# Kernel tuning notes

Hardware: AMD Instinct MI355X
Metric: run time of the kernel (lower is better)

Reference implementation:

```python
import jax, jax.numpy as jnp
import numpy as np

G, N, H = 64, 512, 64          # graphs, nodes/graph, hidden
NT = G * N                     # total nodes
DEG = 32
ET = NT * DEG                  # total edges
KP = int(np.ceil(0.7 * N))     # TopKPooling keep per graph (359)
NP2 = G * KP                   # nodes after pooling
F_IN, NC, NA = 128, 2, 6
seg = jax.ops.segment_sum


def graph_norm(h, batch, num_g, w, b, ms, eps=1e-5):
    cnt = seg(jnp.ones((h.shape[0], 1), h.dtype), batch, num_segments=num_g)
    mean = seg(h, batch, num_segments=num_g) / cnt
    hc = h - ms * mean[batch]
    var = seg(hc * hc, batch, num_segments=num_g) / cnt
    return w * hc / jnp.sqrt(var[batch] + eps) + b


def sage(h, src, tgt, valid, Ws, Wn, b, n_nodes):
    # PyG SAGEConv (mean aggr): out_i = x_i@Ws + mean_{j->i} x_j @ Wn + b
    msg = h[src] * valid[:, None]
    agg = seg(msg, tgt, num_segments=n_nodes)
    deg = seg(valid, tgt, num_segments=n_nodes)
    return h @ Ws + (agg / jnp.maximum(deg, 1.0)[:, None]) @ Wn + b


def setup_inputs() -> dict:
    key = jax.random.key(0)
    ks = jax.random.split(key, 20)
    offs = (jnp.arange(G) * N)[:, None]
    src = (jax.random.randint(ks[0], (G, N * DEG), 0, N) + offs).reshape(-1)
    tgt = (jax.random.randint(ks[1], (G, N * DEG), 0, N) + offs).reshape(-1)
    edge_index = jnp.stack([src, tgt])  # within-graph edges

    def lin(k, fi, fo):
        return jax.random.normal(k, (fi, fo), jnp.float32) / np.sqrt(fi)

    return {
        "x": jax.random.normal(ks[2], (NT, F_IN), jnp.float32),
        "edge_index": edge_index,
        "edge_attr": jax.random.uniform(ks[3], (ET,), jnp.float32),
        "coords": jax.random.normal(ks[4], (NT, 3), jnp.float32),
        "anatomical_class": jax.random.randint(ks[5], (NT,), 0, NA),
        "Bk_table": jax.random.normal(ks[6], (NA, H * H), jnp.float32) * 0.05,
        "pos_W": lin(ks[7], 3, H), "pos_b": jnp.zeros((H,), jnp.float32),
        "W1_self": lin(ks[8], F_IN, H), "W1_neigh": lin(ks[9], F_IN, H),
        "b1": jnp.zeros((H,), jnp.float32),
        "gn1_w": jnp.ones((H,), jnp.float32), "gn1_b": jnp.zeros((H,), jnp.float32),
        "gn1_ms": jnp.ones((H,), jnp.float32),
        "pool_p": jax.random.normal(ks[10], (H,), jnp.float32),
        "W2_self": lin(ks[11], H, H), "W2_neigh": lin(ks[12], H, H),
        "b2": jnp.zeros((H,), jnp.float32),
        "gn2_w": jnp.ones((H,), jnp.float32), "gn2_b": jnp.zeros((H,), jnp.float32),
        "gn2_ms": jnp.ones((H,), jnp.float32),
        "lin1_W": lin(ks[13], 3 * H, H), "lin1_b": jnp.zeros((H,), jnp.float32),
        "lin2_W": lin(ks[14], H, NC), "lin2_b": jnp.zeros((NC,), jnp.float32),
    }


def reference(x, edge_index, edge_attr, coords, anatomical_class, Bk_table,
              pos_W, pos_b, W1_self, W1_neigh, b1, gn1_w, gn1_b, gn1_ms,
              pool_p, W2_self, W2_neigh, b2, gn2_w, gn2_b, gn2_ms,
              lin1_W, lin1_b, lin2_W, lin2_b):
    row, col = edge_index[0], edge_index[1]
    batch = jnp.repeat(jnp.arange(G), N)
    # ---- stage 1: anatomical propagation kernel ----
    e = coords @ pos_W + pos_b                                 # [NT, H]
    Ae = seg(edge_attr[:, None] * e[col], row, num_segments=NT)  # SpMM adj @ e
    Bk = Bk_table[anatomical_class].reshape(NT, H, H)
    delta = jnp.einsum('nd,nhd->nh', Ae, Bk)                   # bmm(Ae, Bk^T)
    ones_e = jnp.ones((ET,), x.dtype)
    h = sage(x, row, col, ones_e, W1_self, W1_neigh, b1, NT)
    h = jax.nn.elu(graph_norm(h, batch, G, gn1_w, gn1_b, gn1_ms))
    h = h + delta
    h = jnp.einsum('nij,nj->ni', Bk + delta[:, :, None], h)    # propagate_message
    # ---- TopK pooling (equal-sized graphs) ----
    score = (h @ pool_p) / jnp.linalg.norm(pool_p)
    vals, idx = jax.lax.top_k(score.reshape(G, N), KP)
    perm = (idx + (jnp.arange(G) * N)[:, None]).reshape(-1)    # [NP2]
    h = h[perm] * jnp.tanh(vals).reshape(-1)[:, None]
    batch2 = jnp.repeat(jnp.arange(G), KP)
    node_map = jnp.full((NT,), -1, jnp.int32).at[perm].set(jnp.arange(NP2, dtype=jnp.int32))
    s2, t2 = node_map[row], node_map[col]
    valid = ((s2 >= 0) & (t2 >= 0)).astype(h.dtype)            # masked edge filter
    s2 = jnp.where(s2 >= 0, s2, 0)
    t2 = jnp.where(t2 >= 0, t2, 0)
    # ---- stage 2 ----
    e2 = coords[perm] @ pos_W + pos_b
    Bk2 = Bk_table[anatomical_class[perm]].reshape(NP2, H, H)
    Ae2 = seg(valid[:, None] * e2[t2], s2, num_segments=NP2)   # edge_attr = ones
    delta2 = jnp.einsum('nd,nhd->nh', Ae2, Bk2)
    h = h + delta2
    h = jnp.einsum('nij,nj->ni', Bk2 + delta2[:, :, None], h)
    h = sage(h, s2, t2, valid, W2_self, W2_neigh, b2, NP2)
    h = jax.nn.elu(graph_norm(h, batch2, G, gn2_w, gn2_b, gn2_ms))
    # ---- readout ----
    cnt = seg(jnp.ones((NP2, 1), h.dtype), batch2, num_segments=G)
    hsum = seg(h, batch2, num_segments=G)
    g = jnp.concatenate([hsum / cnt,
                         jax.ops.segment_max(h, batch2, num_segments=G),
                         hsum], axis=1)
    g = jax.nn.relu(g @ lin1_W + lin1_b)
    return jax.nn.log_softmax(g @ lin2_W + lin2_b, axis=1)
```

## Files before the change

kernel.cpp:

```cpp
#include <hip/hip_runtime.h>
#include <math.h>

#define G_    64
#define N_    512
#define H_    64
#define NT_   32768
#define ET_   1048576
#define EPG_  16384
#define KP_   359
#define NP2_  22976
#define FIN_  128
#define ESL_  2048
#define BPB_  (EPG_/ESL_)

__global__ void k_prep(const float* __restrict__ Bk, const float* __restrict__ posW,
                       const float* __restrict__ posb,
                       float* __restrict__ BkT, float* __restrict__ PT) {
    int b = blockIdx.x, t = threadIdx.x;
    if (b < 96) {
        int idx = b * 256 + t;
        int c = idx >> 12, r = idx & 4095;
        int h = r >> 6, d = r & 63;
        BkT[c * 4096 + d * 64 + h] = Bk[c * 4096 + h * 64 + d];
    } else {
        int c = b - 96;
        int i = t >> 6, h = t & 63;
        const float* B = Bk + c * 4096 + h * 64;
        float acc = 0.f;
        for (int d = 0; d < 64; d++) {
            float vd = (i < 3) ? posW[i*64 + d] : posb[d];
            acc += B[d] * vd;
        }
        PT[c*256 + i*64 + h] = acc;
    }
}

__global__ __launch_bounds__(256)
void k_hist(const int* __restrict__ row, const int* __restrict__ col,
            int* __restrict__ histR, int* __restrict__ histC) {
    __shared__ int hr[N_], hc[N_];
    int b = blockIdx.x, g = b >> 3, s = b & (BPB_ - 1);
    int t = threadIdx.x;
    for (int i = t; i < N_; i += 256) { hr[i] = 0; hc[i] = 0; }
    __syncthreads();
    int ebase = g * EPG_ + s * ESL_;
    for (int i = t; i < ESL_; i += 256) {
        atomicAdd(&hr[row[ebase + i] & (N_ - 1)], 1);
        atomicAdd(&hc[col[ebase + i] & (N_ - 1)], 1);
    }
    __syncthreads();
    int nbase = g * N_;
    for (int i = t; i < N_; i += 256) {
        if (hr[i]) atomicAdd(&histR[nbase + i], hr[i]);
        if (hc[i]) atomicAdd(&histC[nbase + i], hc[i]);
    }
}

__global__ __launch_bounds__(256)
void k_scan(const int* __restrict__ histR, const int* __restrict__ histC,
            int* __restrict__ rowptr, int* __restrict__ colptr,
            float* __restrict__ deg, int* __restrict__ nmap) {
    __shared__ int hr[N_], hc[N_];
    int g = blockIdx.x, t = threadIdx.x;
    int nbase = g * N_;
    for (int i = t; i < N_; i += 256) {
        hr[i] = histR[nbase + i];
        int c = histC[nbase + i];
        hc[i] = c;
        deg[nbase + i] = (float)c;
        nmap[nbase + i] = -1;
    }
    __syncthreads();
    int wave = t >> 6, lane = t & 63;
    if (wave < 2) {
        int* h = wave ? hc : hr;
        int base8 = lane * 8;
        int loc[8];
        int tot = 0;
        #pragma unroll
        for (int i = 0; i < 8; i++) { int v = h[base8 + i]; loc[i] = tot; tot += v; }
        int pref = tot;
        for (int off = 1; off < 64; off <<= 1) {
            int u = __shfl_up(pref, off);
            if (lane >= off) pref += u;
        }
        pref -= tot;
        #pragma unroll
        for (int i = 0; i < 8; i++) h[base8 + i] = pref + loc[i];
    }
    __syncthreads();
    int ebase = g * EPG_;
    for (int i = t; i < N_; i += 256) {
        rowptr[nbase + i] = ebase + hr[i];
        colptr[nbase + i] = ebase + hc[i];
    }
    if (g == 0 && t == 0) { rowptr[NT_] = ET_; colptr[NT_] = ET_; }
}

__global__ __launch_bounds__(1024)
void k_scat(const int* __restrict__ row, const int* __restrict__ col,
            const float* __restrict__ ea,
            const int* __restrict__ rowptr, const int* __restrict__ colptr,
            int2* __restrict__ rowcsr, int* __restrict__ colcsr) {
    __shared__ int curR[128], curC[128];
    int g = blockIdx.x >> 2, q = blockIdx.x & 3;
    int t = threadIdx.x;
    int lo = q * 128;
    int nbase = g * N_ + lo;
    if (t < 128) { curR[t] = rowptr[nbase + t]; curC[t] = colptr[nbase + t]; }
    __syncthreads();
    int ebase = g * EPG_;
    for (int i = t; i < EPG_; i += 1024) {
        int rg = row[ebase + i];
        int cg = col[ebase + i];
        int rl = (rg & (N_ - 1)) - lo;
        if ((unsigned)rl < 128u) {
            int pr = atomicAdd(&curR[rl], 1);
            rowcsr[pr] = make_int2(cg, __float_as_int(ea[ebase + i]));
        }
        int cl = (cg & (N_ - 1)) - lo;
        if ((unsigned)cl < 128u) {
            int pc = atomicAdd(&curC[cl], 1);
            colcsr[pc] = rg;
        }
    }
}

__global__ __launch_bounds__(256)
void k_gemm_dual(const float* __restrict__ in, int K,
                 const float* __restrict__ Wa, const float* __restrict__ Wb,
                 const float* __restrict__ bias, const int* __restrict__ permA,
                 float* __restrict__ outA, float* __restrict__ outB) {
    __shared__ float inT[32 * FIN_];
    int row0 = blockIdx.x * 32;
    int t = threadIdx.x;
    for (int idx = t; idx < 32 * K; idx += 256) inT[idx] = in[row0 * K + idx];
    __syncthreads();
    int c = t & 63, rb = t >> 6;
    const float* ip = inT + (rb * 8) * K;
    float aA[8] = {0,0,0,0,0,0,0,0};
    float aB[8] = {0,0,0,0,0,0,0,0};
    for (int k = 0; k < K; k += 4) {
        float wa0 = Wa[(k+0)*64 + c], wa1 = Wa[(k+1)*64 + c];
        float wa2 = Wa[(k+2)*64 + c], wa3 = Wa[(k+3)*64 + c];
        float wb0 = Wb[(k+0)*64 + c], wb1 = Wb[(k+1)*64 + c];
        float wb2 = Wb[(k+2)*64 + c], wb3 = Wb[(k+3)*64 + c];
        #pragma unroll
        for (int r = 0; r < 8; r++) {
            float4 xv = *(const float4*)&ip[r*K + k];
            aA[r] += xv.x*wa0; aB[r] += xv.x*wb0;
            aA[r] += xv.y*wa1; aB[r] += xv.y*wb1;
            aA[r] += xv.z*wa2; aB[r] += xv.z*wb2;
            aA[r] += xv.w*wa3; aB[r] += xv.w*wb3;
        }
    }
    float bv = bias[c];
    #pragma unroll
    for (int r = 0; r < 8; r++) {
        int node = row0 + rb*8 + r;
        int rowA = permA ? permA[node] : node;
        outA[rowA*64 + c] = aA[r];
        outB[node*64 + c] = aB[r] + bv;
    }
}

__global__ __launch_bounds__(256)
void k_edge1f(const int* __restrict__ rowptr, const int2* __restrict__ rcsr,
              const int* __restrict__ colptr, const int* __restrict__ ccsr,
              const float* __restrict__ coords, const float* __restrict__ y,
              float4* __restrict__ nsum, float* __restrict__ agg) {
    int node = blockIdx.x * 4 + (threadIdx.x >> 6);
    int lane = threadIdx.x & 63;
    int rs = rowptr[node], re = rowptr[node + 1];
    float sx = 0.f, sy = 0.f, sz = 0.f, sw = 0.f;
    for (int k = rs + lane; k < re; k += 64) {
        int2 ent = rcsr[k];
        int c = ent.x;
        float w = __int_as_float(ent.y);
        sx += w * coords[c*3+0];
        sy += w * coords[c*3+1];
        sz += w * coords[c*3+2];
        sw += w;
    }
    #pragma unroll
    for (int off = 32; off; off >>= 1) {
        sx += __shfl_xor(sx, off); sy += __shfl_xor(sy, off);
        sz += __shfl_xor(sz, off); sw += __shfl_xor(sw, off);
    }
    if (lane == 0) nsum[node] = make_float4(sx, sy, sz, sw);
    int cs = colptr[node], ce = colptr[node + 1];
    float acc = 0.f;
    #pragma unroll 8
    for (int k = cs; k < ce; k++) {
        int r = ccsr[k];
        acc += y[r*64 + lane];
    }
    agg[node*64 + lane] = acc;
}

__global__ __launch_bounds__(256)
void k_gnstat(const float* __restrict__ hs, const float* __restrict__ agg,
              const float* __restrict__ deg, float* __restrict__ partial,
              int NPG, int CH, int npc) {
    __shared__ float r1[256], r2[256];
    int b = blockIdx.x;
    int g = b / CH, chunk = b % CH;
    int t = threadIdx.x, c = t & 63, grp = t >> 6;
    int n0 = chunk * npc;
    int nend = min(n0 + npc, NPG);
    float s1 = 0.f, s2 = 0.f;
    for (int n = n0 + grp; n < nend; n += 4) {
        int node = g * NPG + n;
        float v = hs[node*64 + c] + agg[node*64 + c] / fmaxf(deg[node], 1.f);
        s1 += v; s2 += v * v;
    }
    r1[t] = s1; r2[t] = s2;
    __syncthreads();
    if (grp == 0) {
        partial[b*128 + c]      = r1[c] + r1[64+c] + r1[128+c] + r1[192+c];
        partial[b*128 + 64 + c] = r2[c] + r2[64+c] + r2[128+c] + r2[192+c];
    }
}

__global__ void k_gnfin(const float* __restrict__ partial, const float* __restrict__ ms,
                        int CH, int NPG,
                        float* __restrict__ mval, float* __restrict__ istdv) {
    int g = blockIdx.x, t = threadIdx.x;
    float s1 = 0.f, s2 = 0.f;
    for (int i = 0; i < CH; i++) {
        s1 += partial[(g*CH + i)*128 + t];
        s2 += partial[(g*CH + i)*128 + 64 + t];
    }
    float m = s1 / (float)NPG, q = s2 / (float)NPG, msv = ms[t];
    float var = q - msv * m * m * (2.f - msv);
    mval[g*64 + t]  = msv * m;
    istdv[g*64 + t] = rsqrtf(var + 1e-5f);
}

__global__ __launch_bounds__(256)
void k_gnprop(const float* __restrict__ hself, const float* __restrict__ agg,
              const float* __restrict__ deg,
              const float* __restrict__ mval, const float* __restrict__ istdv,
              const float* __restrict__ w, const float* __restrict__ b,
              const float4* __restrict__ nsum, const int* __restrict__ cls,
              const float* __restrict__ PT, const float* __restrict__ BkT,
              float* __restrict__ out) {
    __shared__ float hT[256];
    int t = threadIdx.x;
    int node = blockIdx.x * 4 + (t >> 6);
    int lane = t & 63;
    int g = node >> 9;
    float4 s4 = nsum[node];
    int c = cls[node];
    const float* P = PT + c * 256;
    float d = s4.x*P[lane] + s4.y*P[64+lane] + s4.z*P[128+lane] + s4.w*P[192+lane];
    float v = hself[node*64 + lane] + agg[node*64 + lane] / fmaxf(deg[node], 1.f);
    v = w[lane] * (v - mval[g*64 + lane]) * istdv[g*64 + lane] + b[lane];
    v = v > 0.f ? v : expm1f(v);
    v += d;
    hT[t] = v;
    __syncthreads();
    float ssum = v;
    #pragma unroll
    for (int off = 32; off; off >>= 1) ssum += __shfl_xor(ssum, off);
    const float* B  = BkT + c * 4096;
    const float* hv = hT + (t & ~63);
    float acc = 0.f;
    #pragma unroll 8
    for (int j = 0; j < 64; j++) acc += B[j*64 + lane] * hv[j];
    out[node*64 + lane] = acc + d * ssum;
}

__global__ void k_topk(const float* __restrict__ hp, const float* __restrict__ p,
                       const int* __restrict__ cls,
                       int* __restrict__ perm, float* __restrict__ tanhv,
                       int* __restrict__ node_map, int* __restrict__ class2) {
    __shared__ float key[N_];
    __shared__ int   idxS[N_];
    __shared__ float pS[64];
    __shared__ float nrm;
    int g = blockIdx.x, t = threadIdx.x;
    if (t < 64) pS[t] = p[t];
    __syncthreads();
    if (t == 0) {
        float s = 0.f;
        for (int i = 0; i < 64; i++) s += pS[i] * pS[i];
        nrm = sqrtf(s);
    }
    __syncthreads();
    {
        float acc = 0.f;
        const float* hv = hp + (size_t)(g*N_ + t) * 64;
        for (int cdx = 0; cdx < 64; cdx++) acc += hv[cdx] * pS[cdx];
        key[t]  = acc / nrm;
        idxS[t] = t;
    }
    __syncthreads();
    for (int k = 2; k <= N_; k <<= 1) {
        for (int j = k >> 1; j > 0; j >>= 1) {
            int i = t, ixj = i ^ j;
            if (ixj > i) {
                float ki = key[i], kj = key[ixj];
                int   ii = idxS[i], ij = idxS[ixj];
                bool before = (ki > kj) || (ki == kj && ii < ij);
                bool dir = ((i & k) == 0);
                if (dir ? !before : before) {
                    key[i] = kj; key[ixj] = ki;
                    idxS[i] = ij; idxS[ixj] = ii;
                }
            }
            __syncthreads();
        }
    }
    if (t < KP_) {
        int orig  = idxS[t];
        int gnode = g * N_ + orig;
        int pj    = g * KP_ + t;
        perm[pj]     = gnode;
        tanhv[pj]    = tanhf(key[t]);
        node_map[gnode] = pj;
        class2[pj]   = cls[gnode];
    }
}

__global__ __launch_bounds__(256)
void k_s2prop(const int* __restrict__ rowptr, const int2* __restrict__ rcsr,
              const int* __restrict__ colptr, const int* __restrict__ ccsr,
              const int* __restrict__ perm, const int* __restrict__ nmap,
              const float* __restrict__ coords,
              const float* __restrict__ hp, const float* __restrict__ tanhv,
              const int* __restrict__ cls2,
              const float* __restrict__ PT, const float* __restrict__ BkT,
              float* __restrict__ out, float* __restrict__ deg2) {
    __shared__ float hT[256];
    int t = threadIdx.x;
    int j = blockIdx.x * 4 + (t >> 6);
    int lane = t & 63;
    int orig = perm[j];
    int rs = rowptr[orig], re = rowptr[orig + 1];
    float sx = 0.f, sy = 0.f, sz = 0.f, sw = 0.f;
    for (int k = rs + lane; k < re; k += 64) {
        int c = rcsr[k].x;
        if (nmap[c] >= 0) {
            sx += coords[c*3+0]; sy += coords[c*3+1]; sz += coords[c*3+2];
            sw += 1.f;
        }
    }
    int cs = colptr[orig], ce = colptr[orig + 1];
    float dg = 0.f;
    for (int k = cs + lane; k < ce; k += 64) {
        if (nmap[ccsr[k]] >= 0) dg += 1.f;
    }
    #pragma unroll
    for (int off = 32; off; off >>= 1) {
        sx += __shfl_xor(sx, off); sy += __shfl_xor(sy, off);
        sz += __shfl_xor(sz, off); sw += __shfl_xor(sw, off);
        dg += __shfl_xor(dg, off);
    }
    if (lane == 0) deg2[j] = dg;
    int c = cls2[j];
    const float* P = PT + c * 256;
    float d = sx*P[lane] + sy*P[64+lane] + sz*P[128+lane] + sw*P[192+lane];
    float v = hp[orig*64 + lane] * tanhv[j] + d;
    hT[t] = v;
    __syncthreads();
    float ssum = v;
    #pragma unroll
    for (int off = 32; off; off >>= 1) ssum += __shfl_xor(ssum, off);
    const float* B  = BkT + c * 4096;
    const float* hv = hT + (t & ~63);
    float acc = 0.f;
    #pragma unroll 8
    for (int jj = 0; jj < 64; jj++) acc += B[jj*64 + lane] * hv[jj];
    out[j*64 + lane] = acc + d * ssum;
}

__global__ __launch_bounds__(256)
void k_gagg2(const int* __restrict__ colptr, const int* __restrict__ ccsr,
             const int* __restrict__ perm, const float* __restrict__ y2full,
             float* __restrict__ agg2) {
    int j = blockIdx.x * 4 + (threadIdx.x >> 6);
    int lane = threadIdx.x & 63;
    int orig = perm[j];
    int start = colptr[orig], end = colptr[orig + 1];
    float acc = 0.f;
    #pragma unroll 8
    for (int k = start; k < end; k++) {
        int r = ccsr[k];
        acc += y2full[r*64 + lane];
    }
    agg2[j*64 + lane] = acc;
}

__global__ __launch_bounds__(256)
void k_gnrd(const float* __restrict__ hs, const float* __restrict__ agg,
            const float* __restrict__ deg2,
            const float* __restrict__ mval, const float* __restrict__ istdv,
            const float* __restrict__ w, const float* __restrict__ b,
            float* __restrict__ part, int CH, int npc) {
    __shared__ float r1[256], r2[256];
    int blk = blockIdx.x;
    int g = blk / CH, chunk = blk % CH;
    int t = threadIdx.x, c = t & 63, grp = t >> 6;
    int n0 = chunk * npc, nend = min(n0 + npc, KP_);
    float mv = mval[g*64 + c], is = istdv[g*64 + c], wv = w[c], bv = b[c];
    float s = 0.f, m = -1e30f;
    for (int n = n0 + grp; n < nend; n += 4) {
        int node = g * KP_ + n;
        float v = hs[node*64 + c] + agg[node*64 + c] / fmaxf(deg2[node], 1.f);
        v = wv * (v - mv) * is + bv;
        v = v > 0.f ? v : expm1f(v);
        s += v; m = fmaxf(m, v);
    }
    r1[t] = s; r2[t] = m;
    __syncthreads();
    if (grp == 0) {
        part[blk*128 + c]      = r1[c] + r1[64+c] + r1[128+c] + r1[192+c];
        part[blk*128 + 64 + c] = fmaxf(fmaxf(r2[c], r2[64+c]), fmaxf(r2[128+c], r2[192+c]));
    }
}

__global__ void k_rfin(const float* __restrict__ part, int CH,
                       const float* __restrict__ l1W, const float* __restrict__ l1b,
                       const float* __restrict__ l2W, const float* __restrict__ l2b,
                       float* __restrict__ out) {
    __shared__ float gv[192], rS[64];
    int g = blockIdx.x, t = threadIdx.x;
    float s = 0.f, m = -1e30f;
    for (int i = 0; i < CH; i++) {
        s += part[(g*CH + i)*128 + t];
        m = fmaxf(m, part[(g*CH + i)*128 + 64 + t]);
    }
    gv[t] = s / (float)KP_;
    gv[64 + t] = m;
    gv[128 + t] = s;
    __syncthreads();
    float acc = l1b[t];
    for (int k = 0; k < 192; k++) acc += gv[k] * l1W[k*64 + t];
    rS[t] = fmaxf(acc, 0.f);
    __syncthreads();
    if (t == 0) {
        float l0 = l2b[0], l1v = l2b[1];
        for (int hh = 0; hh < 64; hh++) { l0 += rS[hh]*l2W[hh*2+0]; l1v += rS[hh]*l2W[hh*2+1]; }
        float mx  = fmaxf(l0, l1v);
        float lse = mx + logf(expf(l0 - mx) + expf(l1v - mx));
        out[g*2 + 0] = l0  - lse;
        out[g*2 + 1] = l1v - lse;
    }
}

extern "C" void kernel_launch(void* const* d_in, const int* in_sizes, int n_in,
                              void* d_out, int out_size, void* d_ws, size_t ws_size,
                              hipStream_t stream) {
    const float* x      = (const float*)d_in[0];
    const int*   eidx   = (const int*)  d_in[1];
    const float* eattr  = (const float*)d_in[2];
    const float* coords = (const float*)d_in[3];
    const int*   acls   = (const int*)  d_in[4];
    const float* BkTab  = (const float*)d_in[5];
    const float* posW   = (const float*)d_in[6];
    const float* posb   = (const float*)d_in[7];
    const float* W1s    = (const float*)d_in[8];
    const float* W1n    = (const float*)d_in[9];
    const float* b1     = (const float*)d_in[10];
    const float* gn1w   = (const float*)d_in[11];
    const float* gn1b   = (const float*)d_in[12];
    const float* gn1ms  = (const float*)d_in[13];
    const float* poolp  = (const float*)d_in[14];
    const float* W2s    = (const float*)d_in[15];
    const float* W2n    = (const float*)d_in[16];
    const float* b2     = (const float*)d_in[17];
    const float* gn2w   = (const float*)d_in[18];
    const float* gn2b   = (const float*)d_in[19];
    const float* gn2ms  = (const float*)d_in[20];
    const float* l1W    = (const float*)d_in[21];
    const float* l1b    = (const float*)d_in[22];
    const float* l2W    = (const float*)d_in[23];
    const float* l2b    = (const float*)d_in[24];

    const int* row  = eidx;
    const int* colp = eidx + ET_;

    float* W = (float*)d_ws;
    const size_t NTH = (size_t)NT_ * 64;
    float* b0    = W;
    float* b1buf = W + 1*NTH;
    float* b2buf = W + 2*NTH;
    float* b3buf = W + 3*NTH;
    float* p = W + 4*NTH;
    int2*  rowcsr = (int2*)p;        p += 2*(size_t)ET_;
    int*   colcsr = (int*)p;         p += ET_;
    int*   rowptr = (int*)p;         p += NT_ + 8;
    int*   colptr = (int*)p;         p += NT_ + 8;
    int*   histR  = (int*)p;         p += NT_;
    int*   histC  = (int*)p;         p += NT_;
    float* deg    = p;               p += NT_;
    float* deg2   = p;               p += NP2_;
    float* tanhv  = p;               p += NP2_;
    int*   perm   = (int*)p;         p += NP2_;
    int*   nmap   = (int*)p;         p += NT_;
    int*   cls2   = (int*)p;         p += NP2_;
    float* BkT    = p;               p += 6 * 4096;
    float* PT     = p;               p += 6 * 256;
    float* meanv  = p;               p += G_ * 64;
    float* istdv  = p;               p += G_ * 64;
    float* partial= p;               p += (size_t)G_ * 8 * 128;
    float4* nsum  = (float4*)b3buf;

    hipMemsetAsync(histR, 0, 2 * NT_ * sizeof(int), stream);
    k_prep     <<<102,     256,  0, stream>>>(BkTab, posW, posb, BkT, PT);
    k_hist     <<<G_*BPB_, 256,  0, stream>>>(row, colp, histR, histC);
    k_scan     <<<G_,      256,  0, stream>>>(histR, histC, rowptr, colptr, deg, nmap);
    k_scat     <<<G_*4,    1024, 0, stream>>>(row, colp, eattr, rowptr, colptr,
                                              rowcsr, colcsr);

    k_gemm_dual<<<NT_/32,  256, 0, stream>>>(x, FIN_, W1n, W1s, b1, nullptr,
                                             b0 , b1buf );
    k_edge1f   <<<NT_/4,   256, 0, stream>>>(rowptr, rowcsr, colptr, colcsr,
                                             coords, b0 , nsum, b2buf );
    k_gnstat   <<<G_*8,    256, 0, stream>>>(b1buf , b2buf , deg,
                                             partial, N_, 8, 64);
    k_gnfin    <<<G_,      64,  0, stream>>>(partial, gn1ms, 8, N_, meanv, istdv);
    k_gnprop   <<<NT_/4,   256, 0, stream>>>(b1buf , b2buf , deg,
                                             meanv, istdv, gn1w, gn1b,
                                             nsum, acls, PT, BkT,
                                             b1buf );
    k_topk     <<<G_,      512, 0, stream>>>(b1buf , poolp, acls,
                                             perm, tanhv, nmap, cls2);

    k_s2prop   <<<NP2_/4,  256, 0, stream>>>(rowptr, rowcsr, colptr, colcsr,
                                             perm, nmap, coords,
                                             b1buf , tanhv, cls2, PT, BkT,
                                             b2buf , deg2);
    hipMemsetAsync(b0, 0, NTH * sizeof(float), stream);
    k_gemm_dual<<<NP2_/32, 256, 0, stream>>>(b2buf , 64, W2n, W2s, b2, perm,
                                             b0 , b3buf );
    k_gagg2    <<<NP2_/4,  256, 0, stream>>>(colptr, colcsr, perm, b0 ,
                                             b1buf );
    k_gnstat   <<<G_*6,    256, 0, stream>>>(b3buf , b1buf , deg2,
                                             partial, KP_, 6, 60);
    k_gnfin    <<<G_,      64,  0, stream>>>(partial, gn2ms, 6, KP_, meanv, istdv);
    k_gnrd     <<<G_*6,    256, 0, stream>>>(b3buf , b1buf , deg2,
                                             meanv, istdv, gn2w, gn2b,
                                             partial, 6, 60);
    k_rfin     <<<G_,      64,  0, stream>>>(partial, 6, l1W, l1b, l2W, l2b,
                                             (float*)d_out);
}
```

Before: 343.8 us.

## Fuse small kernels, drop memsets, remap pooled column CSR in top-k

The histogram kernel is merged with the Bk transpose/prep kernel and now writes per-slice histograms that the scan sums, which removes a memset and the global atomics. Both graph-norm finalize kernels are folded into their consumers, each of which recomputes mean and inverse std from the partial sums. Top-k now builds a remapped column CSR (ccsr2) that points into compact pooled indices, with a zeroed sentinel row at NP2. This lets the second GEMM write unpermuted rows and removes the full-buffer memset. The cost is redundant stats recomputation in every block and an extra pass over edges inside the per-graph top-k kernel.

```diff
diff --git a/kernel.cpp b/kernel.cpp
--- a/kernel.cpp
+++ b/kernel.cpp
@@ -13,17 +13,36 @@
 #define ESL_  2048
 #define BPB_  (EPG_/ESL_)
 
-__global__ void k_prep(const float* __restrict__ Bk, const float* __restrict__ posW,
-                       const float* __restrict__ posb,
-                       float* __restrict__ BkT, float* __restrict__ PT) {
+__global__ __launch_bounds__(256)
+void k_histprep(const int* __restrict__ row, const int* __restrict__ col,
+                int* __restrict__ histR8, int* __restrict__ histC8,
+                const float* __restrict__ Bk, const float* __restrict__ posW,
+                const float* __restrict__ posb,
+                float* __restrict__ BkT, float* __restrict__ PT) {
     int b = blockIdx.x, t = threadIdx.x;
-    if (b < 96) {
-        int idx = b * 256 + t;
+    if (b < G_ * BPB_) {
+        __shared__ int hr[N_], hc[N_];
+        int g = b >> 3, s = b & (BPB_ - 1);
+        for (int i = t; i < N_; i += 256) { hr[i] = 0; hc[i] = 0; }
+        __syncthreads();
+        int ebase = g * EPG_ + s * ESL_;
+        for (int i = t; i < ESL_; i += 256) {
+            atomicAdd(&hr[row[ebase + i] & (N_ - 1)], 1);
+            atomicAdd(&hc[col[ebase + i] & (N_ - 1)], 1);
+        }
+        __syncthreads();
+        int sbase = (g * BPB_ + s) * N_;
+        for (int i = t; i < N_; i += 256) {
+            histR8[sbase + i] = hr[i];
+            histC8[sbase + i] = hc[i];
+        }
+    } else if (b < G_ * BPB_ + 96) {
+        int idx = (b - G_ * BPB_) * 256 + t;
         int c = idx >> 12, r = idx & 4095;
         int h = r >> 6, d = r & 63;
         BkT[c * 4096 + d * 64 + h] = Bk[c * 4096 + h * 64 + d];
     } else {
-        int c = b - 96;
+        int c = b - (G_ * BPB_ + 96);
         int i = t >> 6, h = t & 63;
         const float* B = Bk + c * 4096 + h * 64;
         float acc = 0.f;
@@ -36,38 +55,21 @@
 }
 
 __global__ __launch_bounds__(256)
-void k_hist(const int* __restrict__ row, const int* __restrict__ col,
-            int* __restrict__ histR, int* __restrict__ histC) {
-    __shared__ int hr[N_], hc[N_];
-    int b = blockIdx.x, g = b >> 3, s = b & (BPB_ - 1);
-    int t = threadIdx.x;
-    for (int i = t; i < N_; i += 256) { hr[i] = 0; hc[i] = 0; }
-    __syncthreads();
-    int ebase = g * EPG_ + s * ESL_;
-    for (int i = t; i < ESL_; i += 256) {
-        atomicAdd(&hr[row[ebase + i] & (N_ - 1)], 1);
-        atomicAdd(&hc[col[ebase + i] & (N_ - 1)], 1);
-    }
-    __syncthreads();
-    int nbase = g * N_;
-    for (int i = t; i < N_; i += 256) {
-        if (hr[i]) atomicAdd(&histR[nbase + i], hr[i]);
-        if (hc[i]) atomicAdd(&histC[nbase + i], hc[i]);
-    }
-}
-
-__global__ __launch_bounds__(256)
-void k_scan(const int* __restrict__ histR, const int* __restrict__ histC,
+void k_scan(const int* __restrict__ histR8, const int* __restrict__ histC8,
             int* __restrict__ rowptr, int* __restrict__ colptr,
             float* __restrict__ deg, int* __restrict__ nmap) {
     __shared__ int hr[N_], hc[N_];
     int g = blockIdx.x, t = threadIdx.x;
     int nbase = g * N_;
     for (int i = t; i < N_; i += 256) {
-        hr[i] = histR[nbase + i];
-        int c = histC[nbase + i];
-        hc[i] = c;
-        deg[nbase + i] = (float)c;
+        int sr = 0, sc = 0;
+        #pragma unroll
+        for (int s = 0; s < BPB_; s++) {
+            sr += histR8[(g * BPB_ + s) * N_ + i];
+            sc += histC8[(g * BPB_ + s) * N_ + i];
+        }
+        hr[i] = sr; hc[i] = sc;
+        deg[nbase + i] = (float)sc;
         nmap[nbase + i] = -1;
     }
     __syncthreads();
@@ -129,7 +131,7 @@
 __global__ __launch_bounds__(256)
 void k_gemm_dual(const float* __restrict__ in, int K,
                  const float* __restrict__ Wa, const float* __restrict__ Wb,
-                 const float* __restrict__ bias, const int* __restrict__ permA,
+                 const float* __restrict__ bias,
                  float* __restrict__ outA, float* __restrict__ outB) {
     __shared__ float inT[32 * FIN_];
     int row0 = blockIdx.x * 32;
@@ -158,8 +160,7 @@
     #pragma unroll
     for (int r = 0; r < 8; r++) {
         int node = row0 + rb*8 + r;
-        int rowA = permA ? permA[node] : node;
-        outA[rowA*64 + c] = aA[r];
+        outA[node*64 + c] = aA[r];
         outB[node*64 + c] = aB[r] + bv;
     }
 }
@@ -222,25 +223,10 @@
     }
 }
 
-__global__ void k_gnfin(const float* __restrict__ partial, const float* __restrict__ ms,
-                        int CH, int NPG,
-                        float* __restrict__ mval, float* __restrict__ istdv) {
-    int g = blockIdx.x, t = threadIdx.x;
-    float s1 = 0.f, s2 = 0.f;
-    for (int i = 0; i < CH; i++) {
-        s1 += partial[(g*CH + i)*128 + t];
-        s2 += partial[(g*CH + i)*128 + 64 + t];
-    }
-    float m = s1 / (float)NPG, q = s2 / (float)NPG, msv = ms[t];
-    float var = q - msv * m * m * (2.f - msv);
-    mval[g*64 + t]  = msv * m;
-    istdv[g*64 + t] = rsqrtf(var + 1e-5f);
-}
-
 __global__ __launch_bounds__(256)
 void k_gnprop(const float* __restrict__ hself, const float* __restrict__ agg,
-              const float* __restrict__ deg,
-              const float* __restrict__ mval, const float* __restrict__ istdv,
+              const float* __restrict__ deg, const float* __restrict__ partial,
+              const float* __restrict__ ms,
               const float* __restrict__ w, const float* __restrict__ b,
               const float4* __restrict__ nsum, const int* __restrict__ cls,
               const float* __restrict__ PT, const float* __restrict__ BkT,
@@ -249,13 +235,23 @@
     int t = threadIdx.x;
     int node = blockIdx.x * 4 + (t >> 6);
     int lane = t & 63;
-    int g = node >> 9;
+    int g = (blockIdx.x * 4) >> 9;
+    float s1 = 0.f, s2 = 0.f;
+    #pragma unroll
+    for (int i = 0; i < 8; i++) {
+        s1 += partial[(g*8 + i)*128 + lane];
+        s2 += partial[(g*8 + i)*128 + 64 + lane];
+    }
+    float m  = s1 / (float)N_, q = s2 / (float)N_, msv = ms[lane];
+    float var = q - msv * m * m * (2.f - msv);
+    float mval = msv * m;
+    float istd = rsqrtf(var + 1e-5f);
     float4 s4 = nsum[node];
     int c = cls[node];
     const float* P = PT + c * 256;
     float d = s4.x*P[lane] + s4.y*P[64+lane] + s4.z*P[128+lane] + s4.w*P[192+lane];
     float v = hself[node*64 + lane] + agg[node*64 + lane] / fmaxf(deg[node], 1.f);
-    v = w[lane] * (v - mval[g*64 + lane]) * istdv[g*64 + lane] + b[lane];
+    v = w[lane] * (v - mval) * istd + b[lane];
     v = v > 0.f ? v : expm1f(v);
     v += d;
     hT[t] = v;
@@ -271,15 +267,19 @@
     out[node*64 + lane] = acc + d * ssum;
 }
 
-__global__ void k_topk(const float* __restrict__ hp, const float* __restrict__ p,
-                       const int* __restrict__ cls,
-                       int* __restrict__ perm, float* __restrict__ tanhv,
-                       int* __restrict__ node_map, int* __restrict__ class2) {
+__global__ __launch_bounds__(512)
+void k_topk(const float* __restrict__ hp, const float* __restrict__ p,
+            const int* __restrict__ cls, const int* __restrict__ ccsr,
+            int* __restrict__ perm, float* __restrict__ tanhv,
+            int* __restrict__ node_map, int* __restrict__ class2,
+            int* __restrict__ ccsr2) {
     __shared__ float key[N_];
     __shared__ int   idxS[N_];
+    __shared__ int   lmap[N_];
     __shared__ float pS[64];
     __shared__ float nrm;
     int g = blockIdx.x, t = threadIdx.x;
+    lmap[t] = -1;
     if (t < 64) pS[t] = p[t];
     __syncthreads();
     if (t == 0) {
@@ -320,6 +320,13 @@
         tanhv[pj]    = tanhf(key[t]);
         node_map[gnode] = pj;
         class2[pj]   = cls[gnode];
+        lmap[orig]   = pj;
+    }
+    __syncthreads();
+    int ebase = g * EPG_;
+    for (int k = t; k < EPG_; k += 512) {
+        int mm = lmap[ccsr[ebase + k] & (N_ - 1)];
+        ccsr2[ebase + k] = (mm >= 0) ? mm : NP2_;
     }
 }
 
@@ -331,11 +338,13 @@
               const float* __restrict__ hp, const float* __restrict__ tanhv,
               const int* __restrict__ cls2,
               const float* __restrict__ PT, const float* __restrict__ BkT,
-              float* __restrict__ out, float* __restrict__ deg2) {
+              float* __restrict__ out, float* __restrict__ deg2,
+              float* __restrict__ y2zero) {
     __shared__ float hT[256];
     int t = threadIdx.x;
     int j = blockIdx.x * 4 + (t >> 6);
     int lane = t & 63;
+    if (blockIdx.x == 0 && t < 64) y2zero[t] = 0.f;
     int orig = perm[j];
     int rs = rowptr[orig], re = rowptr[orig + 1];
     float sx = 0.f, sy = 0.f, sz = 0.f, sw = 0.f;
@@ -376,8 +385,8 @@
 }
 
 __global__ __launch_bounds__(256)
-void k_gagg2(const int* __restrict__ colptr, const int* __restrict__ ccsr,
-             const int* __restrict__ perm, const float* __restrict__ y2full,
+void k_gagg2(const int* __restrict__ colptr, const int* __restrict__ ccsr2,
+             const int* __restrict__ perm, const float* __restrict__ y2,
              float* __restrict__ agg2) {
     int j = blockIdx.x * 4 + (threadIdx.x >> 6);
     int lane = threadIdx.x & 63;
@@ -386,24 +395,34 @@
     float acc = 0.f;
     #pragma unroll 8
     for (int k = start; k < end; k++) {
-        int r = ccsr[k];
-        acc += y2full[r*64 + lane];
+        int r = ccsr2[k];
+        acc += y2[r*64 + lane];
     }
     agg2[j*64 + lane] = acc;
 }
 
 __global__ __launch_bounds__(256)
 void k_gnrd(const float* __restrict__ hs, const float* __restrict__ agg,
-            const float* __restrict__ deg2,
-            const float* __restrict__ mval, const float* __restrict__ istdv,
+            const float* __restrict__ deg2, const float* __restrict__ statsP,
+            const float* __restrict__ ms,
             const float* __restrict__ w, const float* __restrict__ b,
-            float* __restrict__ part, int CH, int npc) {
+            float* __restrict__ readP) {
     __shared__ float r1[256], r2[256];
     int blk = blockIdx.x;
-    int g = blk / CH, chunk = blk % CH;
+    int g = blk / 6, chunk = blk % 6;
     int t = threadIdx.x, c = t & 63, grp = t >> 6;
-    int n0 = chunk * npc, nend = min(n0 + npc, KP_);
-    float mv = mval[g*64 + c], is = istdv[g*64 + c], wv = w[c], bv = b[c];
+    float s1 = 0.f, s2 = 0.f;
+    #pragma unroll
+    for (int i = 0; i < 6; i++) {
+        s1 += statsP[(g*6 + i)*128 + c];
+        s2 += statsP[(g*6 + i)*128 + 64 + c];
+    }
+    float mean = s1 / (float)KP_, q = s2 / (float)KP_, msv = ms[c];
+    float var = q - msv * mean * mean * (2.f - msv);
+    float mv = msv * mean;
+    float is = rsqrtf(var + 1e-5f);
+    float wv = w[c], bv = b[c];
+    int n0 = chunk * 60, nend = min(n0 + 60, KP_);
     float s = 0.f, m = -1e30f;
     for (int n = n0 + grp; n < nend; n += 4) {
         int node = g * KP_ + n;
@@ -415,8 +434,8 @@
     r1[t] = s; r2[t] = m;
     __syncthreads();
     if (grp == 0) {
-        part[blk*128 + c]      = r1[c] + r1[64+c] + r1[128+c] + r1[192+c];
-        part[blk*128 + 64 + c] = fmaxf(fmaxf(r2[c], r2[64+c]), fmaxf(r2[128+c], r2[192+c]));
+        readP[blk*128 + c]      = r1[c] + r1[64+c] + r1[128+c] + r1[192+c];
+        readP[blk*128 + 64 + c] = fmaxf(fmaxf(r2[c], r2[64+c]), fmaxf(r2[128+c], r2[192+c]));
     }
 }
 
@@ -490,10 +509,11 @@
     float* p = W + 4*NTH;
     int2*  rowcsr = (int2*)p;        p += 2*(size_t)ET_;
     int*   colcsr = (int*)p;         p += ET_;
+    int*   ccsr2  = (int*)p;         p += ET_;
     int*   rowptr = (int*)p;         p += NT_ + 8;
     int*   colptr = (int*)p;         p += NT_ + 8;
-    int*   histR  = (int*)p;         p += NT_;
-    int*   histC  = (int*)p;         p += NT_;
+    int*   histR8 = (int*)p;         p += NT_ * BPB_ / 1;
+    int*   histC8 = (int*)p;         p += NT_ * BPB_ / 1;
     float* deg    = p;               p += NT_;
     float* deg2   = p;               p += NP2_;
     float* tanhv  = p;               p += NP2_;
@@ -502,47 +522,42 @@
     int*   cls2   = (int*)p;         p += NP2_;
     float* BkT    = p;               p += 6 * 4096;
     float* PT     = p;               p += 6 * 256;
-    float* meanv  = p;               p += G_ * 64;
-    float* istdv  = p;               p += G_ * 64;
-    float* partial= p;               p += (size_t)G_ * 8 * 128;
+    float* statsP = p;               p += (size_t)G_ * 8 * 128;
+    float* readP  = p;               p += (size_t)G_ * 6 * 128;
     float4* nsum  = (float4*)b3buf;
 
-    hipMemsetAsync(histR, 0, 2 * NT_ * sizeof(int), stream);
-    k_prep     <<<102,     256,  0, stream>>>(BkTab, posW, posb, BkT, PT);
-    k_hist     <<<G_*BPB_, 256,  0, stream>>>(row, colp, histR, histC);
-    k_scan     <<<G_,      256,  0, stream>>>(histR, histC, rowptr, colptr, deg, nmap);
+    k_histprep <<<G_*BPB_ + 102, 256, 0, stream>>>(row, colp, histR8, histC8,
+                                                   BkTab, posW, posb, BkT, PT);
+    k_scan     <<<G_,      256,  0, stream>>>(histR8, histC8, rowptr, colptr, deg, nmap);
     k_scat     <<<G_*4,    1024, 0, stream>>>(row, colp, eattr, rowptr, colptr,
                                               rowcsr, colcsr);
 
-    k_gemm_dual<<<NT_/32,  256, 0, stream>>>(x, FIN_, W1n, W1s, b1, nullptr,
+    k_gemm_dual<<<NT_/32,  256, 0, stream>>>(x, FIN_, W1n, W1s, b1,
                                              b0 , b1buf );
     k_edge1f   <<<NT_/4,   256, 0, stream>>>(rowptr, rowcsr, colptr, colcsr,
                                              coords, b0 , nsum, b2buf );
     k_gnstat   <<<G_*8,    256, 0, stream>>>(b1buf , b2buf , deg,
-                                             partial, N_, 8, 64);
-    k_gnfin    <<<G_,      64,  0, stream>>>(partial, gn1ms, 8, N_, meanv, istdv);
+                                             statsP, N_, 8, 64);
     k_gnprop   <<<NT_/4,   256, 0, stream>>>(b1buf , b2buf , deg,
-                                             meanv, istdv, gn1w, gn1b,
+                                             statsP, gn1ms, gn1w, gn1b,
                                              nsum, acls, PT, BkT,
                                              b1buf );
-    k_topk     <<<G_,      512, 0, stream>>>(b1buf , poolp, acls,
-                                             perm, tanhv, nmap, cls2);
+    k_topk     <<<G_,      512, 0, stream>>>(b1buf , poolp, acls, colcsr,
+                                             perm, tanhv, nmap, cls2, ccsr2);
 
     k_s2prop   <<<NP2_/4,  256, 0, stream>>>(rowptr, rowcsr, colptr, colcsr,
                                              perm, nmap, coords,
                                              b1buf , tanhv, cls2, PT, BkT,
-                                             b2buf , deg2);
-    hipMemsetAsync(b0, 0, NTH * sizeof(float), stream);
-    k_gemm_dual<<<NP2_/32, 256, 0, stream>>>(b2buf , 64, W2n, W2s, b2, perm,
+                                             b2buf , deg2,
+                                             b0 + (size_t)NP2_ * 64 );
+    k_gemm_dual<<<NP2_/32, 256, 0, stream>>>(b2buf , 64, W2n, W2s, b2,
                                              b0 , b3buf );
-    k_gagg2    <<<NP2_/4,  256, 0, stream>>>(colptr, colcsr, perm, b0 ,
+    k_gagg2    <<<NP2_/4,  256, 0, stream>>>(colptr, ccsr2, perm, b0 ,
                                              b1buf );
     k_gnstat   <<<G_*6,    256, 0, stream>>>(b3buf , b1buf , deg2,
-                                             partial, KP_, 6, 60);
-    k_gnfin    <<<G_,      64,  0, stream>>>(partial, gn2ms, 6, KP_, meanv, istdv);
+                                             statsP, KP_, 6, 60);
     k_gnrd     <<<G_*6,    256, 0, stream>>>(b3buf , b1buf , deg2,
-                                             meanv, istdv, gn2w, gn2b,
-                                             partial, 6, 60);
-    k_rfin     <<<G_,      64,  0, stream>>>(partial, 6, l1W, l1b, l2W, l2b,
+                                             statsP, gn2ms, gn2w, gn2b, readP);
+    k_rfin     <<<G_,      64,  0, stream>>>(readP, 6, l1W, l1b, l2W, l2b,
                                              (float*)d_out);
 }
```

Measured after the change: 335.2 us. 1.03x faster.
